# Performance work log

Hardware: AMD Instinct MI355X
Metric: run time of the kernel (lower is better)

## Reference

```python
import math
import jax, jax.numpy as jnp
import numpy as np

NTYPE, C, H, E = 3, 256, 8, 32  # n_embd=256, n_head=8, edge_dim=32
A1 = 16  # aux_x1 feature dim (aux_x2 dim = E - A1)


def setup_inputs() -> dict:
    key = jax.random.key(0)
    ks = jax.random.split(key, 16)
    B, T1, T2 = 8, 128, 256
    s = 0.02
    return {
        "x1": jax.random.normal(ks[0], (B, T1, C), jnp.float32),
        "x2": jax.random.normal(ks[1], (B, T2, C), jnp.float32),
        "aux_x1": jax.random.normal(ks[2], (B, T1, A1), jnp.float32),
        "aux_x2": jax.random.normal(ks[3], (B, T2, E - A1), jnp.float32),
        "masks": jax.random.randint(ks[4], (NTYPE, B, T1, T2), 0, 2, jnp.int32),
        # per-type linear params, stored (in, out) so y = x @ W + b
        "Wq": jax.random.normal(ks[5], (NTYPE, C, C), jnp.float32) * s,
        "bq": jnp.zeros((NTYPE, C), jnp.float32),
        "Wk": jax.random.normal(ks[6], (NTYPE, C + E, C), jnp.float32) * s,
        "bk": jnp.zeros((NTYPE, C), jnp.float32),
        "Wv": jax.random.normal(ks[7], (NTYPE, C + E, C), jnp.float32) * s,
        "bv": jnp.zeros((NTYPE, C), jnp.float32),
        "Wp": jax.random.normal(ks[8], (NTYPE, C, C), jnp.float32) * s,
        "bp": jnp.zeros((NTYPE, C), jnp.float32),
    }


def _aux_attn(x1, x2, aux_x1, aux_x2, mask, Wq, bq, Wk, bk, Wv, bv, Wp, bp):
    """One AuxCrossAttention type. mask: (B,T1,T2) int."""
    B, T1, _ = x1.shape
    T2 = x2.shape[1]
    hd = C // H
    scale = 1.0 / math.sqrt(hd)

    q = x1 @ Wq + bq  # (B,T1,C)
    # k/v over aug_x2 = [x2 | aux_x1 | aux_x2]; split the linear instead of
    # materializing the (B,T1,T2,C+E) concat (same math by linearity).
    Wk_x, Wk_a1, Wk_a2 = Wk[:C], Wk[C:C + A1], Wk[C + A1:]
    Wv_x, Wv_a1, Wv_a2 = Wv[:C], Wv[C:C + A1], Wv[C + A1:]
    k = (x2 @ Wk_x + aux_x2 @ Wk_a2 + bk)[:, None] + (aux_x1 @ Wk_a1)[:, :, None]  # (B,T1,T2,C)
    v = (x2 @ Wv_x + aux_x2 @ Wv_a2 + bv)[:, None] + (aux_x1 @ Wv_a1)[:, :, None]  # (B,T1,T2,C)

    qh = q.reshape(B, T1, H, hd)
    kh = k.reshape(B, T1, T2, H, hd)
    vh = v.reshape(B, T1, T2, H, hd)

    att = jnp.einsum("bthd,btshd->bhts", qh, kh) * scale  # (B,H,T1,T2)
    valid = (mask != 0)[:, None]  # (B,1,T1,T2)
    att = jnp.where(valid, att, -jnp.inf)
    all_masked = (mask == 0).all(-1)  # (B,T1)
    att = jnp.where(all_masked[:, None, :, None], 0.0, att)
    f = jnp.finfo(att.dtype)
    att = jnp.nan_to_num(att, nan=0.0, posinf=f.max, neginf=f.min)
    att = jax.nn.softmax(att, axis=-1)

    y = jnp.einsum("bhts,btshd->bthd", att, vh).reshape(B, T1, C)
    return y @ Wp + bp


def reference(x1, x2, aux_x1, aux_x2, masks, Wq, bq, Wk, bk, Wv, bv, Wp, bp):
    resid = jnp.zeros_like(x1)
    for i in range(NTYPE):
        resid = resid + _aux_attn(x1, x2, aux_x1, aux_x2, masks[i],
                                  Wq[i], bq[i], Wk[i], bk[i], Wv[i], bv[i], Wp[i], bp[i])
    return resid
```

## Files before the change

### kernel.cpp

```cpp
#include <hip/hip_runtime.h>
#include <hip/hip_bf16.h>

#define NC 256
#define HD 32

typedef __attribute__((ext_vector_type(8))) short short8;
typedef __attribute__((ext_vector_type(4))) short short4v;
typedef __attribute__((ext_vector_type(4))) float f32x4;

#define QSC (0.17677669529663687f * 1.4426950408889634f)

__device__ __forceinline__ unsigned short f2bf(float f) {
    union { float f; unsigned u; } v; v.f = f;
    unsigned r = v.u + 0x7fffu + ((v.u >> 16) & 1u);
    return (unsigned short)(r >> 16);
}
__device__ __forceinline__ short8 cvt8(float4 a, float4 b) {
    short8 s;
    s[0] = (short)f2bf(a.x); s[1] = (short)f2bf(a.y);
    s[2] = (short)f2bf(a.z); s[3] = (short)f2bf(a.w);
    s[4] = (short)f2bf(b.x); s[5] = (short)f2bf(b.y);
    s[6] = (short)f2bf(b.z); s[7] = (short)f2bf(b.w);
    return s;
}

__global__ __launch_bounds__(256) void prep(
    const float* __restrict__ x1, const float* __restrict__ x2,
    const float* __restrict__ ax1, const float* __restrict__ ax2,
    const int* __restrict__ masks,
    const float* __restrict__ Wq, const float* __restrict__ Wk,
    const float* __restrict__ Wv, const float* __restrict__ Wp,
    short* __restrict__ x1b, short* __restrict__ A2, short* __restrict__ ax1p,
    unsigned int* __restrict__ mb,
    short* __restrict__ WqT, short* __restrict__ WkT, short* __restrict__ WvT,
    short* __restrict__ WpT)
{
    const int bx = blockIdx.x, tid = threadIdx.x;
    const short8 zero8 = {0, 0, 0, 0, 0, 0, 0, 0};

    if (bx < 64) {
        const size_t base = ((size_t)bx * 256 + tid) * 16;
        const float* p = x1 + base;
        float4 a = *(const float4*)p,       b = *(const float4*)(p + 4);
        float4 c = *(const float4*)(p + 8), d = *(const float4*)(p + 12);
        *(short8*)&x1b[base]     = cvt8(a, b);
        *(short8*)&x1b[base + 8] = cvt8(c, d);
    } else if (bx < 352) {
        const int g = (bx - 64) * 256 + tid;
        const int row = g / 36, c8 = g - row * 36;
        short8 s;
        if (c8 < 32) {
            const float* p = x2 + (size_t)row * 256 + c8 * 8;
            s = cvt8(*(const float4*)p, *(const float4*)(p + 4));
        } else if (c8 < 34) {
            const float* p = ax2 + (size_t)row * 16 + (c8 - 32) * 8;
            s = cvt8(*(const float4*)p, *(const float4*)(p + 4));
        } else {
            s = zero8;
        }
        *(short8*)&A2[(size_t)row * 288 + c8 * 8] = s;
    } else if (bx < 356) {
        const int row = (bx - 352) * 256 + tid;
        const float* p = ax1 + (size_t)row * 16;
        float4 a = *(const float4*)p,       b = *(const float4*)(p + 4);
        float4 c = *(const float4*)(p + 8), d = *(const float4*)(p + 12);
        short* o = ax1p + (size_t)row * 32;
        *(short8*)o        = cvt8(a, b);
        *(short8*)(o + 8)  = cvt8(c, d);
        *(short8*)(o + 16) = zero8;
        *(short8*)(o + 24) = zero8;
    } else if (bx < 548) {
        const int r0 = (bx - 356) * 16;
        const int wave = tid >> 6, lane = tid & 63;
        for (int rr = 0; rr < 16; ++rr) {
            const int row = r0 + rr;
            const int mk = masks[(size_t)row * 256 + tid];
            unsigned long long bal = __ballot(mk != 0);
            if (lane == 0) {
                mb[row * 8 + wave * 2 + 0] = (unsigned int)bal;
                mb[row * 8 + wave * 2 + 1] = (unsigned int)(bal >> 32);
            }
        }
    } else if (bx < 644) {
        const int idx = bx - 548, i = idx >> 5, k8 = idx & 31;
        const int n = tid;
        const float* W = Wq + (size_t)i * 256 * 256;
        short8 s;
#pragma unroll
        for (int j = 0; j < 8; ++j) s[j] = (short)f2bf(W[(size_t)(k8 * 8 + j) * 256 + n]);
        *(short8*)&WqT[(size_t)i * 256 * 256 + (size_t)n * 256 + k8 * 8] = s;
    } else if (bx < 860) {
        const int idx0 = bx - 644;
        const int kv = idx0 / 108, idx = idx0 % 108;
        const int i = idx / 36, k8 = idx % 36;
        const int n = tid;
        const float* W = (kv ? Wv : Wk) + (size_t)i * 288 * 256;
        short* O = (kv ? WvT : WkT) + (size_t)i * 256 * 288;
        short8 s;
#pragma unroll
        for (int j = 0; j < 8; ++j) {
            const int kp = k8 * 8 + j;
            const int src = (kp < 256) ? kp : (kp < 272 ? kp + 16 : -1);
            s[j] = (src >= 0) ? (short)f2bf(W[(size_t)src * 256 + n]) : (short)0;
        }
        *(short8*)&O[(size_t)n * 288 + k8 * 8] = s;
    } else {
        const int idx = bx - 860, i = idx >> 5, k8 = idx & 31;
        const int n = tid;
        const float* W = Wp + (size_t)i * 256 * 256;
        short8 s;
#pragma unroll
        for (int j = 0; j < 8; ++j) s[j] = (short)f2bf(W[(size_t)(k8 * 8 + j) * 256 + n]);
        *(short8*)&WpT[(size_t)i * 256 * 256 + (size_t)n * 256 + k8 * 8] = s;
    }
}

__global__ __launch_bounds__(256) void fused_gemm(
    const short* __restrict__ x1b, const short* __restrict__ A2,
    const short* __restrict__ WqT, const short* __restrict__ WkT,
    const short* __restrict__ WvT, const float* __restrict__ Wv,
    const short* __restrict__ WpT,
    const float* __restrict__ bq, const float* __restrict__ bk,
    const float* __restrict__ bv,
    short* __restrict__ qb, short* __restrict__ kbb,
    short* __restrict__ vbT, short* __restrict__ WeffT)
{
    const int bx = blockIdx.x;
    const int tid = threadIdx.x;
    const int wave = tid >> 6, lane = tid & 63;
    const int qd = lane >> 4, ml = lane & 15;

    if (bx == 480) {
        f32x4 wacc[4];
#pragma unroll
        for (int nt = 0; nt < 4; ++nt) wacc[nt] = {0.f, 0.f, 0.f, 0.f};
        for (int i = 0; i < 3; ++i) {
            const float* Wvp = Wv + (size_t)i * 288 * 256;
            const short* Wpt = WpT + (size_t)i * 256 * 256;
            for (int step = 0; step < 8; ++step) {
                const float* ap = Wvp + (size_t)(256 + ml) * 256 + step * 32 + qd * 8;
                short8 af = cvt8(*(const float4*)ap, *(const float4*)(ap + 4));
#pragma unroll
                for (int nt = 0; nt < 4; ++nt) {
                    const int n = (wave * 4 + nt) * 16 + ml;
                    short8 bf = *(const short8*)&Wpt[(size_t)n * 256 + step * 32 + qd * 8];
                    wacc[nt] = __builtin_amdgcn_mfma_f32_16x16x32_bf16(af, bf, wacc[nt], 0, 0, 0);
                }
            }
        }
#pragma unroll
        for (int nt = 0; nt < 4; ++nt) {
            const int n = (wave * 4 + nt) * 16 + ml;
#pragma unroll
            for (int r = 0; r < 4; ++r) {
                WeffT[n * 32 + qd * 4 + r] = (short)f2bf(wacc[nt][r]);
                WeffT[n * 32 + 16 + qd * 4 + r] = 0;
            }
        }
        return;
    }

    const short *Ab, *Wb;
    const float* bias;
    short* outb;
    int LDA, LDW, nsteps, mode, m0, n0;
    if (bx < 96) {
        const int i = bx >> 5, t = bx & 31;
        m0 = (t >> 1) * 64; n0 = (t & 1) * 128;
        Ab = x1b; LDA = 256; Wb = WqT + (size_t)i * 256 * 256; LDW = 256;
        nsteps = 8; bias = bq + i * 256; outb = qb + (size_t)i * 1024 * 256; mode = 3;
    } else if (bx < 288) {
        const int idx = bx - 96, i = idx >> 6, t = idx & 63;
        m0 = (t >> 1) * 64; n0 = (t & 1) * 128;
        Ab = A2; LDA = 288; Wb = WkT + (size_t)i * 256 * 288; LDW = 288;
        nsteps = 9; bias = bk + i * 256; outb = kbb + (size_t)i * 2048 * 256; mode = 0;
    } else {
        const int idx = bx - 288, i = idx >> 6, t = idx & 63;
        m0 = (t >> 1) * 64; n0 = (t & 1) * 128;
        Ab = A2; LDA = 288; Wb = WvT + (size_t)i * 256 * 288; LDW = 288;
        nsteps = 9; bias = bv + i * 256; outb = vbT + (size_t)i * 256 * 2048; mode = 1;
    }

    const int wy = wave >> 1, wx = wave & 1;

    f32x4 acc[2][4];
#pragma unroll
    for (int a = 0; a < 2; ++a)
#pragma unroll
        for (int b = 0; b < 4; ++b) acc[a][b] = {0.f, 0.f, 0.f, 0.f};

    for (int step = 0; step < nsteps; ++step) {
        short8 af[2], bf[4];
#pragma unroll
        for (int mt = 0; mt < 2; ++mt)
            af[mt] = *(const short8*)&Ab[(size_t)(m0 + wy * 32 + mt * 16 + ml) * LDA + step * 32 + qd * 8];
#pragma unroll
        for (int nt = 0; nt < 4; ++nt)
            bf[nt] = *(const short8*)&Wb[(size_t)(n0 + wx * 64 + nt * 16 + ml) * LDW + step * 32 + qd * 8];
#pragma unroll
        for (int mt = 0; mt < 2; ++mt)
#pragma unroll
            for (int nt = 0; nt < 4; ++nt)
                acc[mt][nt] = __builtin_amdgcn_mfma_f32_16x16x32_bf16(
                    af[mt], bf[nt], acc[mt][nt], 0, 0, 0);
    }

#pragma unroll
    for (int nt = 0; nt < 4; ++nt) {
        const int col = n0 + wx * 64 + nt * 16 + ml;
        const float bsv = bias[col];
#pragma unroll
        for (int mt = 0; mt < 2; ++mt) {
            const int row0 = m0 + wy * 32 + mt * 16 + qd * 4;
            if (mode == 0) {
#pragma unroll
                for (int r = 0; r < 4; ++r)
                    outb[(size_t)(row0 + r) * 256 + col] = (short)f2bf(acc[mt][nt][r] + bsv);
            } else if (mode == 3) {
#pragma unroll
                for (int r = 0; r < 4; ++r)
                    outb[(size_t)(row0 + r) * 256 + col] = (short)f2bf((acc[mt][nt][r] + bsv) * QSC);
            } else {
                short4v s;
                s.x = (short)f2bf(acc[mt][nt][0] + bsv);
                s.y = (short)f2bf(acc[mt][nt][1] + bsv);
                s.z = (short)f2bf(acc[mt][nt][2] + bsv);
                s.w = (short)f2bf(acc[mt][nt][3] + bsv);
                *(short4v*)&outb[(size_t)col * 2048 + row0] = s;
            }
        }
    }
}

__global__ __launch_bounds__(256) void attn_mfma(
    const short* __restrict__ qb, const short* __restrict__ kbb,
    const short* __restrict__ vbT, const unsigned int* __restrict__ mb,
    short* __restrict__ yb)
{
    const int bx = blockIdx.x;
    const int tc = bx & 1, h = (bx >> 1) & 7, b = (bx >> 4) & 7, i = bx >> 7;
    const size_t bb = (size_t)i * 8 + b;

    __shared__ short Ps[4][32 * 16 * 8];

    const int tid = threadIdx.x;
    const int wave = tid >> 6, lane = tid & 63;
    const int ml = lane & 15, qd = lane >> 4;

    const int t = tc * 64 + wave * 16 + ml;
    short8 af = *(const short8*)&qb[(bb * 128 + t) * 256 + h * HD + qd * 8];

    f32x4 sacc[16];
#pragma unroll
    for (int nt = 0; nt < 16; ++nt) sacc[nt] = {0.f, 0.f, 0.f, 0.f};
#pragma unroll
    for (int nt = 0; nt < 16; ++nt) {
        short8 bf = *(const short8*)&kbb[(bb * 256 + nt * 16 + ml) * 256 + h * HD + qd * 8];
        sacc[nt] = __builtin_amdgcn_mfma_f32_16x16x32_bf16(af, bf, sacc[nt], 0, 0, 0);
    }

    const int tb = tc * 64 + wave * 16 + qd * 4;
    uint4 wlo[4], whi[4];
#pragma unroll
    for (int r = 0; r < 4; ++r) {
        const unsigned int* p = mb + (bb * 128 + tb + r) * 8;
        wlo[r] = *(const uint4*)p;
        whi[r] = *(const uint4*)(p + 4);
    }

    f32x4 rs = {0.f, 0.f, 0.f, 0.f};
#pragma unroll
    for (int nt = 0; nt < 16; ++nt) {
#pragma unroll
        for (int r = 0; r < 4; ++r) {
            unsigned int w;
            switch (nt >> 1) {
                case 0: w = wlo[r].x; break; case 1: w = wlo[r].y; break;
                case 2: w = wlo[r].z; break; case 3: w = wlo[r].w; break;
                case 4: w = whi[r].x; break; case 5: w = whi[r].y; break;
                case 6: w = whi[r].z; break; default: w = whi[r].w; break;
            }
            const bool mk = (w >> ((nt & 1) * 16 + ml)) & 1u;
            float e = mk ? __builtin_amdgcn_exp2f(sacc[nt][r]) : 0.f;
            sacc[nt][r] = e;
            rs[r] += e;
        }
    }
#pragma unroll
    for (int off = 1; off <= 8; off <<= 1) {
#pragma unroll
        for (int r = 0; r < 4; ++r) rs[r] += __shfl_xor(rs[r], off);
    }
    f32x4 pinv, pfill;
#pragma unroll
    for (int r = 0; r < 4; ++r) {
        const bool z = (rs[r] == 0.f);
        pinv[r]  = z ? 0.f : 1.f / rs[r];
        pfill[r] = z ? (1.f / 256.f) : 0.f;
    }

    short* Pw = &Ps[wave][0];
#pragma unroll
    for (int nt = 0; nt < 16; ++nt) {
        const int sgrp = 2 * nt + (ml >> 3);
        const int pos = ml & 7;
#pragma unroll
        for (int r = 0; r < 4; ++r) {
            const float p = sacc[nt][r] * pinv[r] + pfill[r];
            Pw[(sgrp * 16 + qd * 4 + r) * 8 + pos] = (short)f2bf(p);
        }
    }

    f32x4 oacc[2];
    oacc[0] = {0.f, 0.f, 0.f, 0.f};
    oacc[1] = {0.f, 0.f, 0.f, 0.f};
    const short* Vb = vbT + (size_t)i * 256 * 2048 + (size_t)b * 256;
#pragma unroll
    for (int ks = 0; ks < 8; ++ks) {
        short8 pa = *(const short8*)&Pw[((ks * 4 + qd) * 16 + ml) * 8];
#pragma unroll
        for (int n2 = 0; n2 < 2; ++n2) {
            short8 vf = *(const short8*)&Vb[(size_t)(h * HD + n2 * 16 + ml) * 2048 + ks * 32 + qd * 8];
            oacc[n2] = __builtin_amdgcn_mfma_f32_16x16x32_bf16(pa, vf, oacc[n2], 0, 0, 0);
        }
    }

#pragma unroll
    for (int n2 = 0; n2 < 2; ++n2) {
        const int d = h * HD + n2 * 16 + ml;
#pragma unroll
        for (int r = 0; r < 4; ++r) {
            const size_t idx = (bb * 128 + tb + r) * 256 + d;
            yb[idx] = (short)f2bf(oacc[n2][r]);
        }
    }
}

__global__ __launch_bounds__(256) void proj2(
    const short* __restrict__ yb, const short* __restrict__ WpT,
    const short* __restrict__ ax1p, const short* __restrict__ WeffT,
    const float* __restrict__ bp, float* __restrict__ out)
{
    const int bx = blockIdx.x;
    const int m0 = (bx >> 2) * 16, n0 = (bx & 3) * 64;
    const int tid = threadIdx.x;
    const int wave = tid >> 6, lane = tid & 63;
    const int qd = lane >> 4, ml = lane & 15;
    const int col = n0 + wave * 16 + ml;

    f32x4 acc = {0.f, 0.f, 0.f, 0.f};

    for (int i = 0; i < 3; ++i) {
        const short* A = yb + (size_t)i * 1024 * 256;
        const short* W = WpT + (size_t)i * 256 * 256;
#pragma unroll
        for (int step = 0; step < 8; ++step) {
            short8 af = *(const short8*)&A[(size_t)(m0 + ml) * 256 + step * 32 + qd * 8];
            short8 bf = *(const short8*)&W[(size_t)col * 256 + step * 32 + qd * 8];
            acc = __builtin_amdgcn_mfma_f32_16x16x32_bf16(af, bf, acc, 0, 0, 0);
        }
    }
    {
        short8 af = *(const short8*)&ax1p[(size_t)(m0 + ml) * 32 + qd * 8];
        short8 bf = *(const short8*)&WeffT[(size_t)col * 32 + qd * 8];
        acc = __builtin_amdgcn_mfma_f32_16x16x32_bf16(af, bf, acc, 0, 0, 0);
    }
    const float b3 = bp[col] + bp[256 + col] + bp[512 + col];
    const int row0 = m0 + qd * 4;
#pragma unroll
    for (int r = 0; r < 4; ++r)
        out[(size_t)(row0 + r) * 256 + col] = acc[r] + b3;
}

extern "C" void kernel_launch(void* const* d_in, const int* in_sizes, int n_in,
                              void* d_out, int out_size, void* d_ws, size_t ws_size,
                              hipStream_t stream)
{
    const float* x1  = (const float*)d_in[0];
    const float* x2  = (const float*)d_in[1];
    const float* ax1 = (const float*)d_in[2];
    const float* ax2 = (const float*)d_in[3];
    const int*   mk  = (const int*)d_in[4];
    const float* Wq  = (const float*)d_in[5];
    const float* bq  = (const float*)d_in[6];
    const float* Wk  = (const float*)d_in[7];
    const float* bk  = (const float*)d_in[8];
    const float* Wv  = (const float*)d_in[9];
    const float* bv  = (const float*)d_in[10];
    const float* Wp  = (const float*)d_in[11];
    const float* bp  = (const float*)d_in[12];

    char* w = (char*)d_ws;
    short* x1b   = (short*)(w + 0);
    short* A2    = (short*)(w + 524288);
    short* ax1p  = (short*)(w + 1703936);
    short* WqT   = (short*)(w + 1769472);
    short* WkT   = (short*)(w + 2162688);
    short* WvT   = (short*)(w + 2605056);
    short* WpT   = (short*)(w + 3047424);
    unsigned int* mbits = (unsigned int*)(w + 3440640);
    short* WeffT = (short*)(w + 3538944);
    short* qb    = (short*)(w + 3555328);
    short* kbb   = (short*)(w + 5128192);
    short* vbT   = (short*)(w + 8273920);
    short* yb    = (short*)(w + 11419648);

    prep<<<dim3(956), 256, 0, stream>>>(x1, x2, ax1, ax2, mk, Wq, Wk, Wv, Wp,
                                        x1b, A2, ax1p, mbits, WqT, WkT, WvT, WpT);
    fused_gemm<<<dim3(481), 256, 0, stream>>>(x1b, A2, WqT, WkT, WvT, Wv, WpT,
                                              bq, bk, bv, qb, kbb, vbT, WeffT);
    attn_mfma<<<dim3(384), 256, 0, stream>>>(qb, kbb, vbT, mbits, yb);
    proj2<<<dim3(256), 256, 0, stream>>>(yb, WpT, ax1p, WeffT, bp, (float*)d_out);
}
```

Before: 130.0 us.

## Fuse QKV projection GEMMs into attention kernel with per-head LDS staging

Merges the separate QKV GEMM kernel and the attention kernel into one kernel. Each block (type, batch, head) computes its own q, k and v head slice into shared memory and then runs masked softmax and PV from LDS. This removes the global write and re-read of q/k/v and one kernel launch. In exchange the grid drops from 481+384 blocks to 193, so there is less parallelism on a chip with many CUs. Each block also serializes three GEMMs before attention, and A2 rows are re-read once per head.

```diff
diff --git a/kernel.cpp b/kernel.cpp
--- a/kernel.cpp
+++ b/kernel.cpp
@@ -115,22 +115,21 @@
     }
 }
 
-__global__ __launch_bounds__(256) void fused_gemm(
+__global__ __launch_bounds__(256) void qkv_attn(
     const short* __restrict__ x1b, const short* __restrict__ A2,
     const short* __restrict__ WqT, const short* __restrict__ WkT,
     const short* __restrict__ WvT, const float* __restrict__ Wv,
     const short* __restrict__ WpT,
     const float* __restrict__ bq, const float* __restrict__ bk,
-    const float* __restrict__ bv,
-    short* __restrict__ qb, short* __restrict__ kbb,
-    short* __restrict__ vbT, short* __restrict__ WeffT)
+    const float* __restrict__ bv, const unsigned int* __restrict__ mb,
+    short* __restrict__ yb, short* __restrict__ WeffT)
 {
-    const int bx = blockIdx.x;
     const int tid = threadIdx.x;
     const int wave = tid >> 6, lane = tid & 63;
     const int qd = lane >> 4, ml = lane & 15;
-
-    if (bx == 480) {
+    const int bx = blockIdx.x;
+
+    if (bx == 192) {
         f32x4 wacc[4];
 #pragma unroll
         for (int nt = 0; nt < 4; ++nt) wacc[nt] = {0.f, 0.f, 0.f, 0.f};
@@ -160,178 +159,206 @@
         return;
     }
 
-    const short *Ab, *Wb;
-    const float* bias;
-    short* outb;
-    int LDA, LDW, nsteps, mode, m0, n0;
-    if (bx < 96) {
-        const int i = bx >> 5, t = bx & 31;
-        m0 = (t >> 1) * 64; n0 = (t & 1) * 128;
-        Ab = x1b; LDA = 256; Wb = WqT + (size_t)i * 256 * 256; LDW = 256;
-        nsteps = 8; bias = bq + i * 256; outb = qb + (size_t)i * 1024 * 256; mode = 3;
-    } else if (bx < 288) {
-        const int idx = bx - 96, i = idx >> 6, t = idx & 63;
-        m0 = (t >> 1) * 64; n0 = (t & 1) * 128;
-        Ab = A2; LDA = 288; Wb = WkT + (size_t)i * 256 * 288; LDW = 288;
-        nsteps = 9; bias = bk + i * 256; outb = kbb + (size_t)i * 2048 * 256; mode = 0;
-    } else {
-        const int idx = bx - 288, i = idx >> 6, t = idx & 63;
-        m0 = (t >> 1) * 64; n0 = (t & 1) * 128;
-        Ab = A2; LDA = 288; Wb = WvT + (size_t)i * 256 * 288; LDW = 288;
-        nsteps = 9; bias = bv + i * 256; outb = vbT + (size_t)i * 256 * 2048; mode = 1;
-    }
-
-    const int wy = wave >> 1, wx = wave & 1;
-
-    f32x4 acc[2][4];
-#pragma unroll
-    for (int a = 0; a < 2; ++a)
-#pragma unroll
-        for (int b = 0; b < 4; ++b) acc[a][b] = {0.f, 0.f, 0.f, 0.f};
-
-    for (int step = 0; step < nsteps; ++step) {
-        short8 af[2], bf[4];
+    const int i = bx >> 6, b = (bx >> 3) & 7, h = bx & 7;
+    const size_t bb = (size_t)i * 8 + b;
+    const int hc = h * 32;
+
+    __shared__ short q_s[128][40];
+    __shared__ short k_s[256][40];
+    __shared__ short vT_s[32][264];
+    __shared__ short P_s[4][4096];
+
+    const short* Wq_i = WqT + (size_t)i * 256 * 256;
+    const short* Wk_i = WkT + (size_t)i * 256 * 288;
+    const short* Wv_i = WvT + (size_t)i * 256 * 288;
+
+    {
+        f32x4 acc[2][2];
 #pragma unroll
         for (int mt = 0; mt < 2; ++mt)
-            af[mt] = *(const short8*)&Ab[(size_t)(m0 + wy * 32 + mt * 16 + ml) * LDA + step * 32 + qd * 8];
-#pragma unroll
-        for (int nt = 0; nt < 4; ++nt)
-            bf[nt] = *(const short8*)&Wb[(size_t)(n0 + wx * 64 + nt * 16 + ml) * LDW + step * 32 + qd * 8];
-#pragma unroll
-        for (int mt = 0; mt < 2; ++mt)
-#pragma unroll
-            for (int nt = 0; nt < 4; ++nt)
-                acc[mt][nt] = __builtin_amdgcn_mfma_f32_16x16x32_bf16(
-                    af[mt], bf[nt], acc[mt][nt], 0, 0, 0);
-    }
-
-#pragma unroll
-    for (int nt = 0; nt < 4; ++nt) {
-        const int col = n0 + wx * 64 + nt * 16 + ml;
-        const float bsv = bias[col];
-#pragma unroll
-        for (int mt = 0; mt < 2; ++mt) {
-            const int row0 = m0 + wy * 32 + mt * 16 + qd * 4;
-            if (mode == 0) {
+#pragma unroll
+            for (int nt = 0; nt < 2; ++nt) acc[mt][nt] = {0.f, 0.f, 0.f, 0.f};
+        for (int step = 0; step < 8; ++step) {
+            short8 af[2], bf[2];
+#pragma unroll
+            for (int mt = 0; mt < 2; ++mt)
+                af[mt] = *(const short8*)&x1b[(size_t)(b * 128 + wave * 32 + mt * 16 + ml) * 256 + step * 32 + qd * 8];
+#pragma unroll
+            for (int nt = 0; nt < 2; ++nt)
+                bf[nt] = *(const short8*)&Wq_i[(size_t)(hc + nt * 16 + ml) * 256 + step * 32 + qd * 8];
+#pragma unroll
+            for (int mt = 0; mt < 2; ++mt)
+#pragma unroll
+                for (int nt = 0; nt < 2; ++nt)
+                    acc[mt][nt] = __builtin_amdgcn_mfma_f32_16x16x32_bf16(af[mt], bf[nt], acc[mt][nt], 0, 0, 0);
+        }
+#pragma unroll
+        for (int nt = 0; nt < 2; ++nt) {
+            const float bsv = bq[i * 256 + hc + nt * 16 + ml];
+#pragma unroll
+            for (int mt = 0; mt < 2; ++mt) {
+                const int r0 = wave * 32 + mt * 16 + qd * 4;
 #pragma unroll
                 for (int r = 0; r < 4; ++r)
-                    outb[(size_t)(row0 + r) * 256 + col] = (short)f2bf(acc[mt][nt][r] + bsv);
-            } else if (mode == 3) {
+                    q_s[r0 + r][nt * 16 + ml] = (short)f2bf((acc[mt][nt][r] + bsv) * QSC);
+            }
+        }
+    }
+
+    {
+        f32x4 acc[4][2];
+#pragma unroll
+        for (int mt = 0; mt < 4; ++mt)
+#pragma unroll
+            for (int nt = 0; nt < 2; ++nt) acc[mt][nt] = {0.f, 0.f, 0.f, 0.f};
+        for (int step = 0; step < 9; ++step) {
+            short8 af[4], bf[2];
+#pragma unroll
+            for (int mt = 0; mt < 4; ++mt)
+                af[mt] = *(const short8*)&A2[(size_t)(b * 256 + wave * 64 + mt * 16 + ml) * 288 + step * 32 + qd * 8];
+#pragma unroll
+            for (int nt = 0; nt < 2; ++nt)
+                bf[nt] = *(const short8*)&Wk_i[(size_t)(hc + nt * 16 + ml) * 288 + step * 32 + qd * 8];
+#pragma unroll
+            for (int mt = 0; mt < 4; ++mt)
+#pragma unroll
+                for (int nt = 0; nt < 2; ++nt)
+                    acc[mt][nt] = __builtin_amdgcn_mfma_f32_16x16x32_bf16(af[mt], bf[nt], acc[mt][nt], 0, 0, 0);
+        }
+#pragma unroll
+        for (int nt = 0; nt < 2; ++nt) {
+            const float bsv = bk[i * 256 + hc + nt * 16 + ml];
+#pragma unroll
+            for (int mt = 0; mt < 4; ++mt) {
+                const int s0 = wave * 64 + mt * 16 + qd * 4;
 #pragma unroll
                 for (int r = 0; r < 4; ++r)
-                    outb[(size_t)(row0 + r) * 256 + col] = (short)f2bf((acc[mt][nt][r] + bsv) * QSC);
-            } else {
+                    k_s[s0 + r][nt * 16 + ml] = (short)f2bf(acc[mt][nt][r] + bsv);
+            }
+        }
+    }
+
+    {
+        f32x4 acc[4][2];
+#pragma unroll
+        for (int mt = 0; mt < 4; ++mt)
+#pragma unroll
+            for (int nt = 0; nt < 2; ++nt) acc[mt][nt] = {0.f, 0.f, 0.f, 0.f};
+        for (int step = 0; step < 9; ++step) {
+            short8 af[4], bf[2];
+#pragma unroll
+            for (int mt = 0; mt < 4; ++mt)
+                af[mt] = *(const short8*)&A2[(size_t)(b * 256 + wave * 64 + mt * 16 + ml) * 288 + step * 32 + qd * 8];
+#pragma unroll
+            for (int nt = 0; nt < 2; ++nt)
+                bf[nt] = *(const short8*)&Wv_i[(size_t)(hc + nt * 16 + ml) * 288 + step * 32 + qd * 8];
+#pragma unroll
+            for (int mt = 0; mt < 4; ++mt)
+#pragma unroll
+                for (int nt = 0; nt < 2; ++nt)
+                    acc[mt][nt] = __builtin_amdgcn_mfma_f32_16x16x32_bf16(af[mt], bf[nt], acc[mt][nt], 0, 0, 0);
+        }
+#pragma unroll
+        for (int nt = 0; nt < 2; ++nt) {
+            const float bsv = bv[i * 256 + hc + nt * 16 + ml];
+#pragma unroll
+            for (int mt = 0; mt < 4; ++mt) {
+                const int s0 = wave * 64 + mt * 16 + qd * 4;
                 short4v s;
                 s.x = (short)f2bf(acc[mt][nt][0] + bsv);
                 s.y = (short)f2bf(acc[mt][nt][1] + bsv);
                 s.z = (short)f2bf(acc[mt][nt][2] + bsv);
                 s.w = (short)f2bf(acc[mt][nt][3] + bsv);
-                *(short4v*)&outb[(size_t)col * 2048 + row0] = s;
-            }
-        }
-    }
-}
-
-__global__ __launch_bounds__(256) void attn_mfma(
-    const short* __restrict__ qb, const short* __restrict__ kbb,
-    const short* __restrict__ vbT, const unsigned int* __restrict__ mb,
-    short* __restrict__ yb)
-{
-    const int bx = blockIdx.x;
-    const int tc = bx & 1, h = (bx >> 1) & 7, b = (bx >> 4) & 7, i = bx >> 7;
-    const size_t bb = (size_t)i * 8 + b;
-
-    __shared__ short Ps[4][32 * 16 * 8];
-
-    const int tid = threadIdx.x;
-    const int wave = tid >> 6, lane = tid & 63;
-    const int ml = lane & 15, qd = lane >> 4;
-
-    const int t = tc * 64 + wave * 16 + ml;
-    short8 af = *(const short8*)&qb[(bb * 128 + t) * 256 + h * HD + qd * 8];
-
-    f32x4 sacc[16];
-#pragma unroll
-    for (int nt = 0; nt < 16; ++nt) sacc[nt] = {0.f, 0.f, 0.f, 0.f};
-#pragma unroll
-    for (int nt = 0; nt < 16; ++nt) {
-        short8 bf = *(const short8*)&kbb[(bb * 256 + nt * 16 + ml) * 256 + h * HD + qd * 8];
-        sacc[nt] = __builtin_amdgcn_mfma_f32_16x16x32_bf16(af, bf, sacc[nt], 0, 0, 0);
-    }
-
-    const int tb = tc * 64 + wave * 16 + qd * 4;
-    uint4 wlo[4], whi[4];
-#pragma unroll
-    for (int r = 0; r < 4; ++r) {
-        const unsigned int* p = mb + (bb * 128 + tb + r) * 8;
-        wlo[r] = *(const uint4*)p;
-        whi[r] = *(const uint4*)(p + 4);
-    }
-
-    f32x4 rs = {0.f, 0.f, 0.f, 0.f};
-#pragma unroll
-    for (int nt = 0; nt < 16; ++nt) {
+                *(short4v*)&vT_s[nt * 16 + ml][s0] = s;
+            }
+        }
+    }
+    __syncthreads();
+
+    short* Pw = &P_s[wave][0];
+    for (int mt = 0; mt < 2; ++mt) {
+        const int t0 = wave * 32 + mt * 16;
+        short8 af = *(const short8*)&q_s[t0 + ml][qd * 8];
+
+        f32x4 sacc[16];
+#pragma unroll
+        for (int nt = 0; nt < 16; ++nt) sacc[nt] = {0.f, 0.f, 0.f, 0.f};
+#pragma unroll
+        for (int nt = 0; nt < 16; ++nt) {
+            short8 bf = *(const short8*)&k_s[nt * 16 + ml][qd * 8];
+            sacc[nt] = __builtin_amdgcn_mfma_f32_16x16x32_bf16(af, bf, sacc[nt], 0, 0, 0);
+        }
+
+        const int tb = t0 + qd * 4;
+        uint4 wlo[4], whi[4];
 #pragma unroll
         for (int r = 0; r < 4; ++r) {
-            unsigned int w;
-            switch (nt >> 1) {
-                case 0: w = wlo[r].x; break; case 1: w = wlo[r].y; break;
-                case 2: w = wlo[r].z; break; case 3: w = wlo[r].w; break;
-                case 4: w = whi[r].x; break; case 5: w = whi[r].y; break;
-                case 6: w = whi[r].z; break; default: w = whi[r].w; break;
-            }
-            const bool mk = (w >> ((nt & 1) * 16 + ml)) & 1u;
-            float e = mk ? __builtin_amdgcn_exp2f(sacc[nt][r]) : 0.f;
-            sacc[nt][r] = e;
-            rs[r] += e;
-        }
-    }
-#pragma unroll
-    for (int off = 1; off <= 8; off <<= 1) {
-#pragma unroll
-        for (int r = 0; r < 4; ++r) rs[r] += __shfl_xor(rs[r], off);
-    }
-    f32x4 pinv, pfill;
-#pragma unroll
-    for (int r = 0; r < 4; ++r) {
-        const bool z = (rs[r] == 0.f);
-        pinv[r]  = z ? 0.f : 1.f / rs[r];
-        pfill[r] = z ? (1.f / 256.f) : 0.f;
-    }
-
-    short* Pw = &Ps[wave][0];
-#pragma unroll
-    for (int nt = 0; nt < 16; ++nt) {
-        const int sgrp = 2 * nt + (ml >> 3);
-        const int pos = ml & 7;
+            const unsigned int* p = mb + (bb * 128 + tb + r) * 8;
+            wlo[r] = *(const uint4*)p;
+            whi[r] = *(const uint4*)(p + 4);
+        }
+
+        f32x4 rs = {0.f, 0.f, 0.f, 0.f};
+#pragma unroll
+        for (int nt = 0; nt < 16; ++nt) {
+#pragma unroll
+            for (int r = 0; r < 4; ++r) {
+                unsigned int w;
+                switch (nt >> 1) {
+                    case 0: w = wlo[r].x; break; case 1: w = wlo[r].y; break;
+                    case 2: w = wlo[r].z; break; case 3: w = wlo[r].w; break;
+                    case 4: w = whi[r].x; break; case 5: w = whi[r].y; break;
+                    case 6: w = whi[r].z; break; default: w = whi[r].w; break;
+                }
+                const bool mk = (w >> ((nt & 1) * 16 + ml)) & 1u;
+                float e = mk ? __builtin_amdgcn_exp2f(sacc[nt][r]) : 0.f;
+                sacc[nt][r] = e;
+                rs[r] += e;
+            }
+        }
+#pragma unroll
+        for (int off = 1; off <= 8; off <<= 1) {
+#pragma unroll
+            for (int r = 0; r < 4; ++r) rs[r] += __shfl_xor(rs[r], off);
+        }
+        f32x4 pinv, pfill;
 #pragma unroll
         for (int r = 0; r < 4; ++r) {
-            const float p = sacc[nt][r] * pinv[r] + pfill[r];
-            Pw[(sgrp * 16 + qd * 4 + r) * 8 + pos] = (short)f2bf(p);
-        }
-    }
-
-    f32x4 oacc[2];
-    oacc[0] = {0.f, 0.f, 0.f, 0.f};
-    oacc[1] = {0.f, 0.f, 0.f, 0.f};
-    const short* Vb = vbT + (size_t)i * 256 * 2048 + (size_t)b * 256;
-#pragma unroll
-    for (int ks = 0; ks < 8; ++ks) {
-        short8 pa = *(const short8*)&Pw[((ks * 4 + qd) * 16 + ml) * 8];
+            const bool z = (rs[r] == 0.f);
+            pinv[r]  = z ? 0.f : 1.f / rs[r];
+            pfill[r] = z ? (1.f / 256.f) : 0.f;
+        }
+
+#pragma unroll
+        for (int nt = 0; nt < 16; ++nt) {
+            const int sgrp = 2 * nt + (ml >> 3);
+            const int pos = ml & 7;
+#pragma unroll
+            for (int r = 0; r < 4; ++r) {
+                const float p = sacc[nt][r] * pinv[r] + pfill[r];
+                Pw[(sgrp * 16 + qd * 4 + r) * 8 + pos] = (short)f2bf(p);
+            }
+        }
+
+        f32x4 oacc[2];
+        oacc[0] = {0.f, 0.f, 0.f, 0.f};
+        oacc[1] = {0.f, 0.f, 0.f, 0.f};
+#pragma unroll
+        for (int ks = 0; ks < 8; ++ks) {
+            short8 pa = *(const short8*)&Pw[((ks * 4 + qd) * 16 + ml) * 8];
+#pragma unroll
+            for (int n2 = 0; n2 < 2; ++n2) {
+                short8 vf = *(const short8*)&vT_s[n2 * 16 + ml][ks * 32 + qd * 8];
+                oacc[n2] = __builtin_amdgcn_mfma_f32_16x16x32_bf16(pa, vf, oacc[n2], 0, 0, 0);
+            }
+        }
+
 #pragma unroll
         for (int n2 = 0; n2 < 2; ++n2) {
-            short8 vf = *(const short8*)&Vb[(size_t)(h * HD + n2 * 16 + ml) * 2048 + ks * 32 + qd * 8];
-            oacc[n2] = __builtin_amdgcn_mfma_f32_16x16x32_bf16(pa, vf, oacc[n2], 0, 0, 0);
-        }
-    }
-
-#pragma unroll
-    for (int n2 = 0; n2 < 2; ++n2) {
-        const int d = h * HD + n2 * 16 + ml;
-#pragma unroll
-        for (int r = 0; r < 4; ++r) {
-            const size_t idx = (bb * 128 + tb + r) * 256 + d;
-            yb[idx] = (short)f2bf(oacc[n2][r]);
+            const int d = hc + n2 * 16 + ml;
+#pragma unroll
+            for (int r = 0; r < 4; ++r)
+                yb[(size_t)(bb * 128 + tb + r) * 256 + d] = (short)f2bf(oacc[n2][r]);
         }
     }
 }
@@ -400,15 +427,11 @@
     short* WpT   = (short*)(w + 3047424);
     unsigned int* mbits = (unsigned int*)(w + 3440640);
     short* WeffT = (short*)(w + 3538944);
-    short* qb    = (short*)(w + 3555328);
-    short* kbb   = (short*)(w + 5128192);
-    short* vbT   = (short*)(w + 8273920);
-    short* yb    = (short*)(w + 11419648);
+    short* yb    = (short*)(w + 3555328);
 
     prep<<<dim3(956), 256, 0, stream>>>(x1, x2, ax1, ax2, mk, Wq, Wk, Wv, Wp,
                                         x1b, A2, ax1p, mbits, WqT, WkT, WvT, WpT);
-    fused_gemm<<<dim3(481), 256, 0, stream>>>(x1b, A2, WqT, WkT, WvT, Wv, WpT,
-                                              bq, bk, bv, qb, kbb, vbT, WeffT);
-    attn_mfma<<<dim3(384), 256, 0, stream>>>(qb, kbb, vbT, mbits, yb);
+    qkv_attn<<<dim3(193), 256, 0, stream>>>(x1b, A2, WqT, WkT, WvT, Wv, WpT,
+                                            bq, bk, bv, mbits, yb, WeffT);
     proj2<<<dim3(256), 256, 0, stream>>>(yb, WpT, ax1p, WeffT, bp, (float*)d_out);
 }
```

After: 115.9 us. 10.9% less time.
